# Kernel optimization log

Measured on AMD Instinct MI355X. Metric: run time of the kernel, lower is better.

The kernel has to match this reference:

```python
import jax, jax.numpy as jnp
import numpy as np

B, C_IN, C_HID, H, W = 4, 512, 512, 64, 64


def setup_inputs() -> dict:
    key = jax.random.key(0)
    ks = jax.random.split(key, 9)
    s_in = 1.0 / np.sqrt(C_IN)
    s_hid = 1.0 / np.sqrt(C_HID)
    return {
        "inp": jax.random.normal(ks[0], (B, C_IN, H, W), dtype=jnp.float32),
        "Wk": jax.random.normal(ks[1], (C_HID, C_IN), dtype=jnp.float32) * s_in,
        "bk": jax.random.normal(ks[2], (C_HID,), dtype=jnp.float32) * 0.01,
        "Wq": jax.random.normal(ks[3], (C_HID, C_IN), dtype=jnp.float32) * s_in,
        "bq": jax.random.normal(ks[4], (C_HID,), dtype=jnp.float32) * 0.01,
        "Wv": jax.random.normal(ks[5], (C_HID, C_IN), dtype=jnp.float32) * s_in,
        "bv": jax.random.normal(ks[6], (C_HID,), dtype=jnp.float32) * 0.01,
        "Wo": jax.random.normal(ks[7], (C_IN, C_HID), dtype=jnp.float32) * s_hid,
        "bo": jax.random.normal(ks[8], (C_IN,), dtype=jnp.float32) * 0.01,
    }


def reference(inp, Wk, bk, Wq, bq, Wv, bv, Wo, bo):
    b, _, h, w = inp.shape
    n = h * w

    def conv1x1(x, Wt, bias):  # 1x1 conv == per-pixel GEMM
        return jnp.einsum('bchw,oc->bohw', x, Wt) + bias[None, :, None, None]

    k = conv1x1(inp, Wk, bk).reshape(b, C_HID, n)   # [B,Ch,N]
    q = conv1x1(inp, Wq, bq).reshape(b, C_HID, n)
    v = conv1x1(inp, Wv, bv).reshape(b, C_HID, n)

    scale = 1.0 / jnp.sqrt(jnp.asarray(C_HID, dtype=jnp.float32))
    # weight[b,i,j] = <key_i, query_j> / sqrt(Ch); softmax over j (dim=2)
    scores = jnp.einsum('bci,bcj->bij', k, q) * scale  # [B,N,N]
    weight = jax.nn.softmax(scores, axis=2)
    # out[b,c,i] = sum_j weight[b,i,j] * v[b,c,j]
    out = jnp.einsum('bij,bcj->bci', weight, v).reshape(b, C_HID, h, w)
    return conv1x1(out, Wo, bo)  # [B,C_in,H,W]
```

## Files before the change

kernel.cpp:

```cpp
#include <hip/hip_runtime.h>
#include <hip/hip_bf16.h>


typedef __attribute__((ext_vector_type(4))) float f32x4;
typedef __attribute__((ext_vector_type(8))) short short8;
typedef __attribute__((ext_vector_type(4))) short short4v;

#define QSCALE 0.06376639774f
#define FENCE asm volatile("" ::: "memory")
#define SBAR  do { FENCE; __builtin_amdgcn_s_barrier(); FENCE; } while (0)
#define LGKM0 asm volatile("s_waitcnt lgkmcnt(0)" ::: "memory")

__device__ __forceinline__ unsigned short f2bf(float f) {
  unsigned u = __builtin_bit_cast(unsigned, f);
  unsigned r = (u + 0x7FFFu + ((u >> 16) & 1u)) >> 16;
  return (unsigned short)r;
}

__device__ __forceinline__ void gll16(const void* g, void* l) {
  __builtin_amdgcn_global_load_lds((const __attribute__((address_space(1))) void*)g,
                                   (__attribute__((address_space(3))) void*)l, 16, 0, 0);
}

#define MFMA_BF16(d, va, vb) \
  d = __builtin_amdgcn_mfma_f32_16x16x32_bf16(va, vb, d, 0, 0, 0)

__device__ __forceinline__ void gemm256_pipe(
    const short* __restrict__ A, int lda,
    const short* __restrict__ B, int ldb,
    int nkt, char* sm, f32x4 (&acc)[8][4]) {
  const int tid = threadIdx.x, w = tid >> 6, lane = tid & 63;
  const int g = lane >> 4, l15 = lane & 15;
  const int wm = w >> 2, wn = w & 3;
  const int swz = (l15 & 7) << 4;
  const int brow = (wn & 1) << 6;
  const char* SAb = sm + (wm << 14);
  const char* SBb = sm + 65536 + ((wn >> 1) << 14);

  auto stageT = [&](int t) {
    if (t >= nkt) return;
    const int buf = t & 1;
#pragma unroll
    for (int mat = 0; mat < 2; ++mat) {
      const short* src = mat ? B : A;
      const int ld = mat ? ldb : lda;
#pragma unroll
      for (int half = 0; half < 2; ++half) {
        char* dst = sm + mat * 65536 + (buf << 15) + (half << 14) + (w << 10);
        const char* gs = (const char*)src + ((size_t)(half * 128) * ld + (size_t)t * 64) * 2;
#pragma unroll
        for (int q = 0; q < 2; ++q) {
          int o = (q << 13) | (w << 10) | (lane << 4);
          int row = o >> 7, cb = (o & 127) ^ ((row & 7) << 4);
          gll16(gs + (size_t)row * (ld * 2) + cb, dst + (q << 13));
        }
      }
    }
  };
  auto rdSlice = [&](short8* af, short8* bf, int ks, int buf) {
    const char* SA = SAb + (buf << 15);
    const char* SB = SBb + (buf << 15);
#pragma unroll
    for (int i = 0; i < 8; ++i)
      af[i] = *(const short8*)(SA + (i * 16 + l15) * 128 + ((ks * 64 + g * 16) ^ swz));
#pragma unroll
    for (int nf = 0; nf < 4; ++nf)
      bf[nf] = *(const short8*)(SB + (brow + nf * 16 + l15) * 128 + ((ks * 64 + g * 16) ^ swz));
  };
  auto mmAll = [&](short8* af, short8* bf) {
    __builtin_amdgcn_s_setprio(1);
#pragma unroll
    for (int i = 0; i < 8; ++i)
#pragma unroll
      for (int nf = 0; nf < 4; ++nf)
        MFMA_BF16(acc[i][nf], af[i], bf[nf]);
    __builtin_amdgcn_s_setprio(0);
  };

  stageT(0); stageT(1);
  asm volatile("s_waitcnt vmcnt(8)" ::: "memory"); SBAR;
  short8 aX[8], bX[4], aY[8], bY[4];
  rdSlice(aX, bX, 0, 0);
  for (int T = 0; T < nkt; ++T) {
    const int buf = T & 1;
    rdSlice(aY, bY, 1, buf);
    mmAll(aX, bX);
    LGKM0; SBAR;
    stageT(T + 2);
    if (T + 1 < nkt) {
      if (T + 2 < nkt) asm volatile("s_waitcnt vmcnt(8)" ::: "memory");
      else             asm volatile("s_waitcnt vmcnt(0)" ::: "memory");
      SBAR;
      rdSlice(aX, bX, 0, buf ^ 1);
    }
    mmAll(aY, bY);
  }
}

__global__ __launch_bounds__(256) void cvt_w_kernel(
    const float* __restrict__ wk, const float* __restrict__ wq,
    const float* __restrict__ wv, const float* __restrict__ wo,
    short* __restrict__ o) {
  int z = blockIdx.y;
  const float* s = (z == 0) ? wk : (z == 1) ? wq : (z == 2) ? wv : wo;
  int i = blockIdx.x * 256 + threadIdx.x;
  float4 f = ((const float4*)s)[i];
  short4v v;
  v[0] = (short)f2bf(f.x); v[1] = (short)f2bf(f.y);
  v[2] = (short)f2bf(f.z); v[3] = (short)f2bf(f.w);
  if (z < 3) {
    *(short4v*)(o + z * 262144 + i * 4) = v;
  } else {
    int idx = i * 4, co = idx >> 9, cc = idx & 511;
    short* base = o + 786432 + co * 1024 + cc;
    *(short4v*)base = v;
    *(short4v*)(base + 512) = v;
  }
}

__global__ __launch_bounds__(256) void transpose_x_kernel(
    const float* __restrict__ inp, short* __restrict__ xt) {
  __shared__ float t[32][33];
  int tx = threadIdx.x, ty = threadIdx.y;
  int n0 = blockIdx.x * 32, c0 = blockIdx.y * 32, b = blockIdx.z;
  const float* src = inp + ((size_t)(b * 512 + c0)) * 4096 + n0;
#pragma unroll
  for (int r = 0; r < 4; ++r) t[ty + r * 8][tx] = src[(ty + r * 8) * 4096 + tx];
  __syncthreads();
  short* dst = xt + ((size_t)((b << 12) + n0)) * 512 + c0;
#pragma unroll
  for (int r = 0; r < 4; ++r) dst[(ty + r * 8) * 512 + tx] = (short)f2bf(t[tx][ty + r * 8]);
}

__global__ __launch_bounds__(512, 2) void kqv256_kernel(
    const short* __restrict__ xt,
    const short* __restrict__ wk, const short* __restrict__ wq, const short* __restrict__ wv,
    const float* __restrict__ bk, const float* __restrict__ bq, const float* __restrict__ bv,
    short* __restrict__ kt, short* __restrict__ qt, short* __restrict__ vc) {
  extern __shared__ char sm[];
  const int bid = blockIdx.x;
  const int xcd = bid & 7, s = bid >> 3;
  const int pg = s / 6, t = s % 6;
  const int panel = pg * 8 + xcd;
  const int z = (t < 4) ? (t >> 1) : 2;
  const short *A, *B;
  int arow0, brow0;
  if (z < 2) {
    arow0 = panel * 256; brow0 = (t & 1) * 256;
    A = xt + (size_t)arow0 * 512;
    B = ((z == 0) ? wk : wq) + (size_t)brow0 * 512;
  } else {
    arow0 = (t - 4) * 256; brow0 = panel * 256;
    A = wv + (size_t)arow0 * 512;
    B = xt + (size_t)brow0 * 512;
  }
  f32x4 acc[8][4] = {};
  gemm256_pipe(A, 512, B, 512, 8, sm, acc);
  const int tid = threadIdx.x, w = tid >> 6, lane = tid & 63;
  const int gq = lane >> 4, l15 = lane & 15;
  const int wm = w >> 2, wn = w & 3;
#pragma unroll
  for (int mf = 0; mf < 8; ++mf)
#pragma unroll
    for (int nf = 0; nf < 4; ++nf)
#pragma unroll
      for (int r = 0; r < 4; ++r) {
        int row = wm * 128 + mf * 16 + gq * 4 + r;
        int col = wn * 64 + nf * 16 + l15;
        float v = acc[mf][nf][r];
        if (z == 0)      kt[(size_t)(arow0 + row) * 512 + brow0 + col] =
                           (short)f2bf((v + bk[brow0 + col]) * QSCALE);
        else if (z == 1) qt[(size_t)(arow0 + row) * 512 + brow0 + col] =
                           (short)f2bf(v + bq[brow0 + col]);
        else             vc[(size_t)(arow0 + row) * 16384 + brow0 + col] =
                           (short)f2bf(v + bv[arow0 + row]);
      }
}

__global__ __launch_bounds__(512, 2) void gemm_s256_kernel(
    const short* __restrict__ kt, const short* __restrict__ qt,
    short* __restrict__ P, float* __restrict__ Lpart) {
  extern __shared__ char sm[];
  const int bid = blockIdx.x;
  const int xcd = bid & 7, s = bid >> 3;
  const int b = xcd >> 1, h = xcd & 1;
  const int jt0 = (s & 7) * 256, i0 = (s >> 3) * 256;
  const short* A = kt + ((size_t)(b << 12) + i0) * 512;
  const short* B = qt + ((size_t)((b << 12) + h * 2048 + jt0)) * 512;
  f32x4 acc[8][4] = {};
  gemm256_pipe(A, 512, B, 512, 8, sm, acc);
  const int tid = threadIdx.x, w = tid >> 6, lane = tid & 63;
  const int gq = lane >> 4, l15 = lane & 15;
  const int wm = w >> 2, wn = w & 3;
  short* Pb = P + (size_t)h * 33554432 +
              ((size_t)((b << 12) + i0 + wm * 128)) * 2048 + jt0 + wn * 64;
  float psum[8][4];
#pragma unroll
  for (int mf = 0; mf < 8; ++mf)
#pragma unroll
    for (int r = 0; r < 4; ++r) psum[mf][r] = 0.f;
#pragma unroll
  for (int mf = 0; mf < 8; ++mf)
#pragma unroll
    for (int nf = 0; nf < 4; ++nf)
#pragma unroll
      for (int r = 0; r < 4; ++r) {
        float p = exp2f(acc[mf][nf][r]);
        psum[mf][r] += p;
        Pb[(size_t)(mf * 16 + gq * 4 + r) * 2048 + nf * 16 + l15] = (short)f2bf(p);
      }
  const int jp = (h * 2048 + jt0 + wn * 64) >> 6;
  float* Lp = Lpart + (((size_t)b * 64 + jp) << 12) + i0 + wm * 128;
#pragma unroll
  for (int mf = 0; mf < 8; ++mf)
#pragma unroll
    for (int r = 0; r < 4; ++r) {
      float ss = psum[mf][r];
      ss += __shfl_xor(ss, 1); ss += __shfl_xor(ss, 2);
      ss += __shfl_xor(ss, 4); ss += __shfl_xor(ss, 8);
      if (l15 == 0) Lp[mf * 16 + gq * 4 + r] = ss;
    }
}

__global__ __launch_bounds__(512, 2) void gemm_pv256_kernel(
    const short* __restrict__ P, const short* __restrict__ vc,
    short* __restrict__ otab) {
  extern __shared__ char sm[];
  const int bid = blockIdx.x;
  const int xcd = bid & 7, s = bid >> 3;
  const int b = xcd >> 1, h = xcd & 1;
  const int c0 = (s & 1) * 256, i0 = (s >> 1) * 256;
  const short* A = P + (size_t)h * 33554432 + ((size_t)((b << 12) + i0)) * 2048;
  const short* B = vc + (size_t)c0 * 16384 + (b << 12) + h * 2048;
  f32x4 acc[8][4] = {};
  gemm256_pipe(A, 2048, B, 16384, 32, sm, acc);
  const int tid = threadIdx.x, w = tid >> 6, lane = tid & 63;
  const int gq = lane >> 4, l15 = lane & 15;
  const int wm = w >> 2, wn = w & 3;
  short* Ob = otab + ((size_t)((b << 12) + i0 + wm * 128)) * 1024 + h * 512 + c0 + wn * 64;
#pragma unroll
  for (int mf = 0; mf < 8; ++mf)
#pragma unroll
    for (int nf = 0; nf < 4; ++nf)
#pragma unroll
      for (int r = 0; r < 4; ++r)
        Ob[(size_t)(mf * 16 + gq * 4 + r) * 1024 + nf * 16 + l15] =
            (short)f2bf(acc[mf][nf][r]);
}

__global__ __launch_bounds__(256) void lred_kernel(
    const float* __restrict__ Lpart, float* __restrict__ linv) {
  int i = blockIdx.x * 256 + threadIdx.x;
  int b = i >> 12;
  float s = 0.f;
#pragma unroll 8
  for (int jp = 0; jp < 64; ++jp) s += Lpart[(((size_t)b * 64 + jp) << 12) + (i & 4095)];
  linv[i] = 1.0f / s;
}

__global__ __launch_bounds__(512, 2) void out256_kernel(
    const short* __restrict__ wdup, const short* __restrict__ otab,
    const float* __restrict__ bo, const float* __restrict__ linv,
    float* __restrict__ out) {
  extern __shared__ char sm[];
  const int bid = blockIdx.x;
  const int xcd = bid & 7, nt = bid >> 3;
  const int b = xcd >> 1, cot = xcd & 1;
  const int arow0 = cot * 256;
  const int bn0 = nt * 256;
  const short* A = wdup + (size_t)arow0 * 1024;
  const short* B = otab + ((size_t)((b << 12) + bn0)) * 1024;
  f32x4 acc[8][4] = {};
  gemm256_pipe(A, 1024, B, 1024, 16, sm, acc);
  const int tid = threadIdx.x, w = tid >> 6, lane = tid & 63;
  const int gq = lane >> 4, l15 = lane & 15;
  const int wm = w >> 2, wn = w & 3;
#pragma unroll
  for (int mf = 0; mf < 8; ++mf) {
    int co = arow0 + wm * 128 + mf * 16 + gq * 4;
#pragma unroll
    for (int nf = 0; nf < 4; ++nf) {
      int nl = bn0 + wn * 64 + nf * 16 + l15;
      float li = linv[(b << 12) + nl];
#pragma unroll
      for (int r = 0; r < 4; ++r)
        out[((size_t)(b * 512 + co + r) << 12) + nl] = acc[mf][nf][r] * li + bo[co + r];
    }
  }
}

extern "C" void kernel_launch(void* const* d_in, const int* in_sizes, int n_in,
                              void* d_out, int out_size, void* d_ws, size_t ws_size,
                              hipStream_t stream) {
  const float* inp = (const float*)d_in[0];
  const float* Wk = (const float*)d_in[1];
  const float* bk = (const float*)d_in[2];
  const float* Wq = (const float*)d_in[3];
  const float* bq = (const float*)d_in[4];
  const float* Wv = (const float*)d_in[5];
  const float* bv = (const float*)d_in[6];
  const float* Wo = (const float*)d_in[7];
  const float* bo = (const float*)d_in[8];
  float* out = (float*)d_out;
  char* ws = (char*)d_ws;
  const size_t MB = 1048576;
  short* kt    = (short*)(ws);
  short* qt    = (short*)(ws + 16 * MB);
  short* vc    = (short*)(ws + 32 * MB);
  short* wb    = (short*)(ws + 48 * MB);
  short* xt    = (short*)(ws + 51 * MB);
  float* Lpart = (float*)(ws + 51 * MB);
  float* linv  = (float*)(ws + 55 * MB);
  short* P     = (short*)(ws + 67 * MB);
  short* otab  = (short*)(ws + 195 * MB);

  (void)in_sizes; (void)n_in; (void)out_size; (void)ws_size;

  hipFuncSetAttribute((const void*)kqv256_kernel,
                      hipFuncAttributeMaxDynamicSharedMemorySize, 131072);
  hipFuncSetAttribute((const void*)gemm_s256_kernel,
                      hipFuncAttributeMaxDynamicSharedMemorySize, 131072);
  hipFuncSetAttribute((const void*)gemm_pv256_kernel,
                      hipFuncAttributeMaxDynamicSharedMemorySize, 131072);
  hipFuncSetAttribute((const void*)out256_kernel,
                      hipFuncAttributeMaxDynamicSharedMemorySize, 131072);

  cvt_w_kernel<<<dim3(256, 4), 256, 0, stream>>>(Wk, Wq, Wv, Wo, wb);
  transpose_x_kernel<<<dim3(128, 16, 4), dim3(32, 8, 1), 0, stream>>>(inp, xt);
  kqv256_kernel<<<384, 512, 131072, stream>>>(
      xt, wb, wb + 262144, wb + 524288, bk, bq, bv, kt, qt, vc);
  gemm_s256_kernel<<<1024, 512, 131072, stream>>>(kt, qt, P, Lpart);
  gemm_pv256_kernel<<<256, 512, 131072, stream>>>(P, vc, otab);
  lred_kernel<<<64, 256, 0, stream>>>(Lpart, linv);
  out256_kernel<<<128, 512, 131072, stream>>>(wb + 786432, otab, bo, linv, out);
}
```

Before: 283.0 us.

## Replace double-buffered 256x256 GEMM tiles with single-buffered 128x256 four-wave tiles

Swaps the 8-wave, 256x256-tile, double-buffered GEMM core for a 4-wave, 128x256-tile version. It uses 48KB of static LDS and a simple load, sync, compute loop with no prefetch. All four GEMM kernels are retiled and their grids doubled, aiming for more blocks per CU and better load balance. The cost is losing the overlap of global loads with MFMA work, plus lower reuse per tile, since the B panel is loaded twice as often.

```diff
diff --git a/kernel.cpp b/kernel.cpp
--- a/kernel.cpp
+++ b/kernel.cpp
@@ -7,9 +7,6 @@
 typedef __attribute__((ext_vector_type(4))) short short4v;
 
 #define QSCALE 0.06376639774f
-#define FENCE asm volatile("" ::: "memory")
-#define SBAR  do { FENCE; __builtin_amdgcn_s_barrier(); FENCE; } while (0)
-#define LGKM0 asm volatile("s_waitcnt lgkmcnt(0)" ::: "memory")
 
 __device__ __forceinline__ unsigned short f2bf(float f) {
   unsigned u = __builtin_bit_cast(unsigned, f);
@@ -25,75 +22,53 @@
 #define MFMA_BF16(d, va, vb) \
   d = __builtin_amdgcn_mfma_f32_16x16x32_bf16(va, vb, d, 0, 0, 0)
 
-__device__ __forceinline__ void gemm256_pipe(
+__device__ __forceinline__ void gemm_fat(
     const short* __restrict__ A, int lda,
     const short* __restrict__ B, int ldb,
     int nkt, char* sm, f32x4 (&acc)[8][4]) {
   const int tid = threadIdx.x, w = tid >> 6, lane = tid & 63;
   const int g = lane >> 4, l15 = lane & 15;
-  const int wm = w >> 2, wn = w & 3;
   const int swz = (l15 & 7) << 4;
-  const int brow = (wn & 1) << 6;
-  const char* SAb = sm + (wm << 14);
-  const char* SBb = sm + 65536 + ((wn >> 1) << 14);
-
-  auto stageT = [&](int t) {
-    if (t >= nkt) return;
-    const int buf = t & 1;
-#pragma unroll
-    for (int mat = 0; mat < 2; ++mat) {
-      const short* src = mat ? B : A;
-      const int ld = mat ? ldb : lda;
-#pragma unroll
-      for (int half = 0; half < 2; ++half) {
-        char* dst = sm + mat * 65536 + (buf << 15) + (half << 14) + (w << 10);
-        const char* gs = (const char*)src + ((size_t)(half * 128) * ld + (size_t)t * 64) * 2;
-#pragma unroll
-        for (int q = 0; q < 2; ++q) {
-          int o = (q << 13) | (w << 10) | (lane << 4);
-          int row = o >> 7, cb = (o & 127) ^ ((row & 7) << 4);
-          gll16(gs + (size_t)row * (ld * 2) + cb, dst + (q << 13));
-        }
+
+  for (int t = 0; t < nkt; ++t) {
+    __syncthreads();
+#pragma unroll
+    for (int reg = 0; reg < 3; ++reg) {
+      const short* src = reg ? B : A;
+      const int ld = reg ? ldb : lda;
+      const int rbase = (reg == 2) ? 128 : 0;
+#pragma unroll
+      for (int pass = 0; pass < 4; ++pass) {
+        int chunk = pass * 4 + w;
+        int o = chunk * 1024 + lane * 16;
+        int row = o >> 7;
+        int cb = (o & 127) ^ ((row & 7) << 4);
+        gll16((const char*)src + (size_t)(rbase + row) * (ld * 2) +
+                  (size_t)t * 128 + cb,
+              sm + reg * 16384 + chunk * 1024);
       }
     }
-  };
-  auto rdSlice = [&](short8* af, short8* bf, int ks, int buf) {
-    const char* SA = SAb + (buf << 15);
-    const char* SB = SBb + (buf << 15);
-#pragma unroll
-    for (int i = 0; i < 8; ++i)
-      af[i] = *(const short8*)(SA + (i * 16 + l15) * 128 + ((ks * 64 + g * 16) ^ swz));
-#pragma unroll
-    for (int nf = 0; nf < 4; ++nf)
-      bf[nf] = *(const short8*)(SB + (brow + nf * 16 + l15) * 128 + ((ks * 64 + g * 16) ^ swz));
-  };
-  auto mmAll = [&](short8* af, short8* bf) {
-    __builtin_amdgcn_s_setprio(1);
-#pragma unroll
-    for (int i = 0; i < 8; ++i)
-#pragma unroll
-      for (int nf = 0; nf < 4; ++nf)
-        MFMA_BF16(acc[i][nf], af[i], bf[nf]);
-    __builtin_amdgcn_s_setprio(0);
-  };
-
-  stageT(0); stageT(1);
-  asm volatile("s_waitcnt vmcnt(8)" ::: "memory"); SBAR;
-  short8 aX[8], bX[4], aY[8], bY[4];
-  rdSlice(aX, bX, 0, 0);
-  for (int T = 0; T < nkt; ++T) {
-    const int buf = T & 1;
-    rdSlice(aY, bY, 1, buf);
-    mmAll(aX, bX);
-    LGKM0; SBAR;
-    stageT(T + 2);
-    if (T + 1 < nkt) {
-      if (T + 2 < nkt) asm volatile("s_waitcnt vmcnt(8)" ::: "memory");
-      else             asm volatile("s_waitcnt vmcnt(0)" ::: "memory");
-      SBAR;
-      rdSlice(aX, bX, 0, buf ^ 1);
+    __syncthreads();
+#pragma unroll
+    for (int ks = 0; ks < 2; ++ks) {
+      short8 a[8], bb[4];
+#pragma unroll
+      for (int i = 0; i < 8; ++i)
+        a[i] = *(const short8*)(sm + (i * 16 + l15) * 128 + ((ks * 64 + g * 16) ^ swz));
+#pragma unroll
+      for (int nf = 0; nf < 4; ++nf) {
+        int r = w * 64 + nf * 16 + l15;
+        bb[nf] = *(const short8*)(sm + 16384 + (r >> 7) * 16384 + (r & 127) * 128 +
+                                  ((ks * 64 + g * 16) ^ swz));
+      }
+      __builtin_amdgcn_s_setprio(1);
+#pragma unroll
+      for (int i = 0; i < 8; ++i)
+#pragma unroll
+        for (int nf = 0; nf < 4; ++nf)
+          MFMA_BF16(acc[i][nf], a[i], bb[nf]);
+      __builtin_amdgcn_s_setprio(0);
     }
-    mmAll(aY, bY);
   }
 }
 
@@ -132,41 +107,42 @@
   for (int r = 0; r < 4; ++r) dst[(ty + r * 8) * 512 + tx] = (short)f2bf(t[tx][ty + r * 8]);
 }
 
-__global__ __launch_bounds__(512, 2) void kqv256_kernel(
+__global__ __launch_bounds__(256, 2) void kqv_kernel(
     const short* __restrict__ xt,
     const short* __restrict__ wk, const short* __restrict__ wq, const short* __restrict__ wv,
     const float* __restrict__ bk, const float* __restrict__ bq, const float* __restrict__ bv,
     short* __restrict__ kt, short* __restrict__ qt, short* __restrict__ vc) {
-  extern __shared__ char sm[];
+  __shared__ char sm[49152];
   const int bid = blockIdx.x;
   const int xcd = bid & 7, s = bid >> 3;
-  const int pg = s / 6, t = s % 6;
-  const int panel = pg * 8 + xcd;
-  const int z = (t < 4) ? (t >> 1) : 2;
+  const int gg = (s / 12) * 8 + xcd;
+  const int t = s % 12;
+  const int z = (t < 8) ? (t >> 2) : 2;
   const short *A, *B;
   int arow0, brow0;
   if (z < 2) {
-    arow0 = panel * 256; brow0 = (t & 1) * 256;
+    arow0 = gg * 256 + ((t >> 1) & 1) * 128;
+    brow0 = (t & 1) * 256;
     A = xt + (size_t)arow0 * 512;
     B = ((z == 0) ? wk : wq) + (size_t)brow0 * 512;
   } else {
-    arow0 = (t - 4) * 256; brow0 = panel * 256;
+    arow0 = (t - 8) * 128;
+    brow0 = gg * 256;
     A = wv + (size_t)arow0 * 512;
     B = xt + (size_t)brow0 * 512;
   }
   f32x4 acc[8][4] = {};
-  gemm256_pipe(A, 512, B, 512, 8, sm, acc);
+  gemm_fat(A, 512, B, 512, 8, sm, acc);
   const int tid = threadIdx.x, w = tid >> 6, lane = tid & 63;
   const int gq = lane >> 4, l15 = lane & 15;
-  const int wm = w >> 2, wn = w & 3;
 #pragma unroll
   for (int mf = 0; mf < 8; ++mf)
 #pragma unroll
     for (int nf = 0; nf < 4; ++nf)
 #pragma unroll
       for (int r = 0; r < 4; ++r) {
-        int row = wm * 128 + mf * 16 + gq * 4 + r;
-        int col = wn * 64 + nf * 16 + l15;
+        int row = mf * 16 + gq * 4 + r;
+        int col = w * 64 + nf * 16 + l15;
         float v = acc[mf][nf][r];
         if (z == 0)      kt[(size_t)(arow0 + row) * 512 + brow0 + col] =
                            (short)f2bf((v + bk[brow0 + col]) * QSCALE);
@@ -177,23 +153,22 @@
       }
 }
 
-__global__ __launch_bounds__(512, 2) void gemm_s256_kernel(
+__global__ __launch_bounds__(256, 2) void gemm_s_kernel(
     const short* __restrict__ kt, const short* __restrict__ qt,
     short* __restrict__ P, float* __restrict__ Lpart) {
-  extern __shared__ char sm[];
+  __shared__ char sm[49152];
   const int bid = blockIdx.x;
   const int xcd = bid & 7, s = bid >> 3;
   const int b = xcd >> 1, h = xcd & 1;
-  const int jt0 = (s & 7) * 256, i0 = (s >> 3) * 256;
-  const short* A = kt + ((size_t)(b << 12) + i0) * 512;
+  const int it = s >> 3, jt = s & 7;
+  const int i0 = it * 128, jt0 = jt * 256;
+  const short* A = kt + ((size_t)((b << 12) + i0)) * 512;
   const short* B = qt + ((size_t)((b << 12) + h * 2048 + jt0)) * 512;
   f32x4 acc[8][4] = {};
-  gemm256_pipe(A, 512, B, 512, 8, sm, acc);
+  gemm_fat(A, 512, B, 512, 8, sm, acc);
   const int tid = threadIdx.x, w = tid >> 6, lane = tid & 63;
   const int gq = lane >> 4, l15 = lane & 15;
-  const int wm = w >> 2, wn = w & 3;
-  short* Pb = P + (size_t)h * 33554432 +
-              ((size_t)((b << 12) + i0 + wm * 128)) * 2048 + jt0 + wn * 64;
+  short* Pb = P + (size_t)h * 33554432 + ((size_t)((b << 12) + i0)) * 2048 + jt0;
   float psum[8][4];
 #pragma unroll
   for (int mf = 0; mf < 8; ++mf)
@@ -207,10 +182,12 @@
       for (int r = 0; r < 4; ++r) {
         float p = exp2f(acc[mf][nf][r]);
         psum[mf][r] += p;
-        Pb[(size_t)(mf * 16 + gq * 4 + r) * 2048 + nf * 16 + l15] = (short)f2bf(p);
-      }
-  const int jp = (h * 2048 + jt0 + wn * 64) >> 6;
-  float* Lp = Lpart + (((size_t)b * 64 + jp) << 12) + i0 + wm * 128;
+        int row = mf * 16 + gq * 4 + r;
+        int col = w * 64 + nf * 16 + l15;
+        Pb[(size_t)row * 2048 + col] = (short)f2bf(p);
+      }
+  const int jp = (h * 2048 + jt0 + w * 64) >> 6;
+  float* Lp = Lpart + (((size_t)b * 64 + jp) << 12) + i0;
 #pragma unroll
   for (int mf = 0; mf < 8; ++mf)
 #pragma unroll
@@ -222,30 +199,32 @@
     }
 }
 
-__global__ __launch_bounds__(512, 2) void gemm_pv256_kernel(
+__global__ __launch_bounds__(256, 2) void gemm_pv_kernel(
     const short* __restrict__ P, const short* __restrict__ vc,
     short* __restrict__ otab) {
-  extern __shared__ char sm[];
+  __shared__ char sm[49152];
   const int bid = blockIdx.x;
   const int xcd = bid & 7, s = bid >> 3;
   const int b = xcd >> 1, h = xcd & 1;
-  const int c0 = (s & 1) * 256, i0 = (s >> 1) * 256;
+  const int it = s >> 1, ct = s & 1;
+  const int i0 = it * 128, c0 = ct * 256;
   const short* A = P + (size_t)h * 33554432 + ((size_t)((b << 12) + i0)) * 2048;
   const short* B = vc + (size_t)c0 * 16384 + (b << 12) + h * 2048;
   f32x4 acc[8][4] = {};
-  gemm256_pipe(A, 2048, B, 16384, 32, sm, acc);
+  gemm_fat(A, 2048, B, 16384, 32, sm, acc);
   const int tid = threadIdx.x, w = tid >> 6, lane = tid & 63;
   const int gq = lane >> 4, l15 = lane & 15;
-  const int wm = w >> 2, wn = w & 3;
-  short* Ob = otab + ((size_t)((b << 12) + i0 + wm * 128)) * 1024 + h * 512 + c0 + wn * 64;
+  short* Ob = otab + ((size_t)((b << 12) + i0)) * 1024 + h * 512 + c0;
 #pragma unroll
   for (int mf = 0; mf < 8; ++mf)
 #pragma unroll
     for (int nf = 0; nf < 4; ++nf)
 #pragma unroll
-      for (int r = 0; r < 4; ++r)
-        Ob[(size_t)(mf * 16 + gq * 4 + r) * 1024 + nf * 16 + l15] =
-            (short)f2bf(acc[mf][nf][r]);
+      for (int r = 0; r < 4; ++r) {
+        int row = mf * 16 + gq * 4 + r;
+        int col = w * 64 + nf * 16 + l15;
+        Ob[(size_t)row * 1024 + col] = (short)f2bf(acc[mf][nf][r]);
+      }
 }
 
 __global__ __launch_bounds__(256) void lred_kernel(
@@ -258,29 +237,30 @@
   linv[i] = 1.0f / s;
 }
 
-__global__ __launch_bounds__(512, 2) void out256_kernel(
+__global__ __launch_bounds__(256, 2) void gemm_out_kernel(
     const short* __restrict__ wdup, const short* __restrict__ otab,
     const float* __restrict__ bo, const float* __restrict__ linv,
     float* __restrict__ out) {
-  extern __shared__ char sm[];
+  __shared__ char sm[49152];
   const int bid = blockIdx.x;
-  const int xcd = bid & 7, nt = bid >> 3;
-  const int b = xcd >> 1, cot = xcd & 1;
-  const int arow0 = cot * 256;
+  const int xcd = bid & 7, s = bid >> 3;
+  const int b = xcd >> 1, ch = xcd & 1;
+  const int cot = ch * 2 + (s & 1);
+  const int nt = s >> 1;
+  const int arow0 = cot * 128;
   const int bn0 = nt * 256;
   const short* A = wdup + (size_t)arow0 * 1024;
   const short* B = otab + ((size_t)((b << 12) + bn0)) * 1024;
   f32x4 acc[8][4] = {};
-  gemm256_pipe(A, 1024, B, 1024, 16, sm, acc);
+  gemm_fat(A, 1024, B, 1024, 16, sm, acc);
   const int tid = threadIdx.x, w = tid >> 6, lane = tid & 63;
   const int gq = lane >> 4, l15 = lane & 15;
-  const int wm = w >> 2, wn = w & 3;
 #pragma unroll
   for (int mf = 0; mf < 8; ++mf) {
-    int co = arow0 + wm * 128 + mf * 16 + gq * 4;
+    int co = arow0 + mf * 16 + gq * 4;
 #pragma unroll
     for (int nf = 0; nf < 4; ++nf) {
-      int nl = bn0 + wn * 64 + nf * 16 + l15;
+      int nl = bn0 + w * 64 + nf * 16 + l15;
       float li = linv[(b << 12) + nl];
 #pragma unroll
       for (int r = 0; r < 4; ++r)
@@ -316,21 +296,12 @@
 
   (void)in_sizes; (void)n_in; (void)out_size; (void)ws_size;
 
-  hipFuncSetAttribute((const void*)kqv256_kernel,
-                      hipFuncAttributeMaxDynamicSharedMemorySize, 131072);
-  hipFuncSetAttribute((const void*)gemm_s256_kernel,
-                      hipFuncAttributeMaxDynamicSharedMemorySize, 131072);
-  hipFuncSetAttribute((const void*)gemm_pv256_kernel,
-                      hipFuncAttributeMaxDynamicSharedMemorySize, 131072);
-  hipFuncSetAttribute((const void*)out256_kernel,
-                      hipFuncAttributeMaxDynamicSharedMemorySize, 131072);
-
   cvt_w_kernel<<<dim3(256, 4), 256, 0, stream>>>(Wk, Wq, Wv, Wo, wb);
   transpose_x_kernel<<<dim3(128, 16, 4), dim3(32, 8, 1), 0, stream>>>(inp, xt);
-  kqv256_kernel<<<384, 512, 131072, stream>>>(
+  kqv_kernel<<<768, 256, 0, stream>>>(
       xt, wb, wb + 262144, wb + 524288, bk, bq, bv, kt, qt, vc);
-  gemm_s256_kernel<<<1024, 512, 131072, stream>>>(kt, qt, P, Lpart);
-  gemm_pv256_kernel<<<256, 512, 131072, stream>>>(P, vc, otab);
+  gemm_s_kernel<<<2048, 256, 0, stream>>>(kt, qt, P, Lpart);
+  gemm_pv_kernel<<<512, 256, 0, stream>>>(P, vc, otab);
   lred_kernel<<<64, 256, 0, stream>>>(Lpart, linv);
-  out256_kernel<<<128, 512, 131072, stream>>>(wb + 786432, otab, bo, linv, out);
-}
+  gemm_out_kernel<<<256, 256, 0, stream>>>(wb + 786432, otab, bo, linv, out);
+}
```

Measured after the change: 274.7 us. 2.9% less time.
